# Kernel tuning notes

Hardware: AMD Instinct MI355X
Metric: run time of the kernel (lower is better)

Reference implementation:

```python
import jax, jax.numpy as jnp
import numpy as np

D_K = 64
EPS = 1e-6


def setup_inputs() -> dict:
    key = jax.random.key(0)
    ks = jax.random.split(key, 6)
    B, S, D2, DV = 4, 2048, 1024, 64
    q = jax.random.normal(ks[0], (B, S, D2), dtype=jnp.float32)
    k = jax.random.normal(ks[1], (B, S, D2), dtype=jnp.float32)
    v = jax.random.normal(ks[2], (B, S, D2), dtype=jnp.float32)
    mask = jax.random.randint(ks[3], (B, S, S), 0, 2) == 1
    V = jax.random.normal(ks[4], (1, DV), dtype=jnp.float32)
    fc_w = jax.random.normal(ks[5], (D2, DV), dtype=jnp.float32) * (1.0 / np.sqrt(DV))
    fc_b = jnp.zeros((D2,), dtype=jnp.float32)
    ln_g = jnp.ones((D2,), dtype=jnp.float32)
    ln_b = jnp.zeros((D2,), dtype=jnp.float32)
    return {"q": q, "k": k, "v": v, "mask": mask, "V": V,
            "fc_w": fc_w, "fc_b": fc_b, "ln_g": ln_g, "ln_b": ln_b}


def _layer_norm(x, g, b):
    mu = jnp.mean(x, axis=-1, keepdims=True)
    var = jnp.var(x, axis=-1, keepdims=True)
    return (x - mu) * jax.lax.rsqrt(var + EPS) * g + b


def reference(q, k, v, mask, V, fc_w, fc_b, ln_g, ln_b):
    residual = q
    qn = _layer_norm(q, ln_g, ln_b)
    # scaled dot-product scores (no softmax in this variant)
    attn = jnp.einsum('bsd,btd->bst', qn / jnp.sqrt(jnp.float32(D_K)), k)
    attn = jnp.where(mask, 0.0, attn)  # masked_fill with 0
    # v_ = V broadcast over (batch, seq, key); attn @ v_ == row-sum outer V
    output = jnp.sum(attn, axis=-1, keepdims=True) * V  # [B,S,d_v]
    output = output @ fc_w.T + fc_b                     # [B,S,2*d_model]
    output = output + residual
    return (output, attn)
```

## Files before the change

kernel.cpp:

```cpp
#include <hip/hip_runtime.h>
#include <hip/hip_bf16.h>
#include <cstdint>

#define S_LEN 2048
#define D2_   1024
#define DV_   64
#define NB_   4

typedef __bf16 bf16x8 __attribute__((ext_vector_type(8)));
typedef float  f32x4  __attribute__((ext_vector_type(4)));

__device__ __forceinline__ unsigned short f2bf(float f) {
  union { float f; unsigned int u; } v; v.f = f;
  unsigned int r = v.u + 0x7fffu + ((v.u >> 16) & 1u);
  return (unsigned short)(r >> 16);
}

__device__ __forceinline__ void async16(const unsigned short* g, unsigned short* l) {
  __builtin_amdgcn_global_load_lds(
      (__attribute__((address_space(1))) void*)g,
      (__attribute__((address_space(3))) void*)l,
      16, 0, 0);
}

__global__ void __launch_bounds__(256) ln_q_kernel(
    const float* __restrict__ q, const float* __restrict__ gam,
    const float* __restrict__ bet, unsigned short* __restrict__ qn) {
  const int row = blockIdx.x;
  const int t = threadIdx.x;
  const float4 x = ((const float4*)(q + (size_t)row * D2_))[t];
  float s  = x.x + x.y + x.z + x.w;
  float ss = x.x * x.x + x.y * x.y + x.z * x.z + x.w * x.w;
  #pragma unroll
  for (int o = 32; o > 0; o >>= 1) { s += __shfl_down(s, o); ss += __shfl_down(ss, o); }
  __shared__ float red[8];
  if ((t & 63) == 0) { red[t >> 6] = s; red[(t >> 6) + 4] = ss; }
  __syncthreads();
  const float tot  = red[0] + red[1] + red[2] + red[3];
  const float tots = red[4] + red[5] + red[6] + red[7];
  const float mu  = tot * (1.0f / D2_);
  const float var = tots * (1.0f / D2_) - mu * mu;
  const float rs  = rsqrtf(var + 1e-6f) * 0.125f;
  const float4 gv = ((const float4*)gam)[t];
  const float4 bv = ((const float4*)bet)[t];
  ushort4 o4;
  o4.x = f2bf((x.x - mu) * rs * gv.x + 0.125f * bv.x);
  o4.y = f2bf((x.y - mu) * rs * gv.y + 0.125f * bv.y);
  o4.z = f2bf((x.z - mu) * rs * gv.z + 0.125f * bv.z);
  o4.w = f2bf((x.w - mu) * rs * gv.w + 0.125f * bv.w);
  ((ushort4*)(qn + (size_t)row * D2_))[t] = o4;
}

__global__ void __launch_bounds__(256) cast_k_kernel(
    const float* __restrict__ k, unsigned short* __restrict__ kb) {
  const size_t i = ((size_t)blockIdx.x * 256 + threadIdx.x) * 8;
  const float4 a = ((const float4*)(k + i))[0];
  const float4 b = ((const float4*)(k + i))[1];
  ushort4 lo, hi;
  lo.x = f2bf(a.x); lo.y = f2bf(a.y); lo.z = f2bf(a.z); lo.w = f2bf(a.w);
  hi.x = f2bf(b.x); hi.y = f2bf(b.y); hi.z = f2bf(b.z); hi.w = f2bf(b.w);
  ((ushort4*)(kb + i))[0] = lo;
  ((ushort4*)(kb + i))[1] = hi;
}

__global__ void __launch_bounds__(256) w2_kernel(
    const float* __restrict__ V, const float* __restrict__ fw,
    float* __restrict__ w2) {
  const int d = blockIdx.x * 256 + threadIdx.x;
  const float4* r  = (const float4*)(fw + (size_t)d * DV_);
  const float4* vv = (const float4*)V;
  float s = 0.f;
  #pragma unroll
  for (int j = 0; j < 16; ++j) {
    const float4 a = r[j], b = vv[j];
    s += a.x * b.x + a.y * b.y + a.z * b.z + a.w * b.w;
  }
  w2[d] = s;
}

__global__ void __launch_bounds__(256) attn_gemm_kernel(
    const unsigned short* __restrict__ qn,
    const unsigned short* __restrict__ kb,
    const int* __restrict__ mask,
    float* __restrict__ attn) {
  __shared__ __align__(16) unsigned short Asm_[128 * 32];
  __shared__ __align__(16) unsigned short Bsm_[128 * 32];

  const int t  = threadIdx.x;
  const int bn = blockIdx.x * 128;
  const int bm = blockIdx.y * 128;
  const int bt = blockIdx.z;

  const unsigned short* gA = qn + ((size_t)bt * S_LEN + bm + (t >> 2)) * D2_ + (t & 3) * 8;
  const unsigned short* gB = kb + ((size_t)bt * S_LEN + bn + (t >> 2)) * D2_ + (t & 3) * 8;
  unsigned short* lA = Asm_ + t * 8;
  unsigned short* lB = Bsm_ + t * 8;

  const int lane = t & 63;
  const int w  = t >> 6;
  const int wm = (w >> 1) * 64;
  const int wn = (w & 1) * 64;
  const int lr = lane & 15;
  const int lg = lane >> 4;

  f32x4 acc[4][4] = {};

  for (int k0 = 0; k0 < D2_; k0 += 32) {
    async16(gA, lA);
    async16(gA + 64 * D2_, lA + 2048);
    async16(gB, lB);
    async16(gB + 64 * D2_, lB + 2048);
    gA += 32; gB += 32;
    __syncthreads();
    bf16x8 af[4], bfv[4];
    #pragma unroll
    for (int f = 0; f < 4; ++f) {
      af[f]  = *(const bf16x8*)(Asm_ + (wm + f * 16 + lr) * 32 + lg * 8);
      bfv[f] = *(const bf16x8*)(Bsm_ + (wn + f * 16 + lr) * 32 + lg * 8);
    }
    #pragma unroll
    for (int fm = 0; fm < 4; ++fm)
      #pragma unroll
      for (int fn = 0; fn < 4; ++fn)
        acc[fm][fn] = __builtin_amdgcn_mfma_f32_16x16x32_bf16(
            af[fm], bfv[fn], acc[fm][fn], 0, 0, 0);
    __syncthreads();
  }

  #pragma unroll
  for (int fm = 0; fm < 4; ++fm) {
    #pragma unroll
    for (int r = 0; r < 4; ++r) {
      const int srow = bm + wm + fm * 16 + lg * 4 + r;
      const size_t off = ((size_t)bt * S_LEN + srow) * S_LEN + bn + wn;
      const int* mrow = mask + off;
      float*    arow = attn + off;
      #pragma unroll
      for (int fn = 0; fn < 4; ++fn) {
        const int c = fn * 16 + lr;
        float vv = acc[fm][fn][r];
        vv = mrow[c] ? 0.0f : vv;
        arow[c] = vv;
      }
    }
  }
}

__global__ void __launch_bounds__(256) out_kernel(
    const float* __restrict__ attn, const float* __restrict__ q,
    const float* __restrict__ w2, const float* __restrict__ fcb,
    float* __restrict__ out) {
  const int row = blockIdx.x;
  const int t = threadIdx.x;
  const float4* ar = (const float4*)(attn + (size_t)row * S_LEN);
  const float4 a = ar[t], b = ar[t + 256];
  float s = a.x + a.y + a.z + a.w + b.x + b.y + b.z + b.w;
  #pragma unroll
  for (int o = 32; o > 0; o >>= 1) s += __shfl_down(s, o);
  __shared__ float red[4];
  if ((t & 63) == 0) red[t >> 6] = s;
  __syncthreads();
  const float rs = red[0] + red[1] + red[2] + red[3];
  const float4 wv = ((const float4*)w2)[t];
  const float4 bv = ((const float4*)fcb)[t];
  const float4 qv = ((const float4*)(q + (size_t)row * D2_))[t];
  float4 o4;
  o4.x = rs * wv.x + bv.x + qv.x;
  o4.y = rs * wv.y + bv.y + qv.y;
  o4.z = rs * wv.z + bv.z + qv.z;
  o4.w = rs * wv.w + bv.w + qv.w;
  ((float4*)(out + (size_t)row * D2_))[t] = o4;
}

extern "C" void kernel_launch(void* const* d_in, const int* in_sizes, int n_in,
                              void* d_out, int out_size, void* d_ws, size_t ws_size,
                              hipStream_t stream) {
  (void)in_sizes; (void)n_in; (void)out_size; (void)ws_size;
  const float* q    = (const float*)d_in[0];
  const float* k    = (const float*)d_in[1];
  const int*   mask = (const int*)d_in[3];
  const float* V    = (const float*)d_in[4];
  const float* fw   = (const float*)d_in[5];
  const float* fcb  = (const float*)d_in[6];
  const float* lg   = (const float*)d_in[7];
  const float* lb   = (const float*)d_in[8];

  float* out  = (float*)d_out;
  float* attn = out + (size_t)NB_ * S_LEN * D2_;

  unsigned short* qn = (unsigned short*)out;
  unsigned short* kb = qn + (size_t)NB_ * S_LEN * D2_;
  float* w2 = (float*)d_ws;

  ln_q_kernel<<<NB_ * S_LEN, 256, 0, stream>>>(q, lg, lb, qn);
  cast_k_kernel<<<(NB_ * S_LEN * D2_) / 2048, 256, 0, stream>>>(k, kb);
  w2_kernel<<<D2_ / 256, 256, 0, stream>>>(V, fw, w2);
  attn_gemm_kernel<<<dim3(S_LEN / 128, S_LEN / 128, NB_), 256, 0, stream>>>(qn, kb, mask, attn);
  out_kernel<<<NB_ * S_LEN, 256, 0, stream>>>(attn, q, w2, fcb, out);
}
```

Before: 297.3 us.

## Double-buffer LDS tiles in attention GEMM and fuse prep kernels

The attention GEMM now ping-pongs between two LDS buffers, issuing async global-to-LDS loads for the next K-slice before computing the current one, and drops the trailing barrier per iteration. The separate layernorm, K-cast and fc-weight-reduction kernels are merged into a single prep kernel to cut launches. This aims to hide global load latency behind MFMA work, at the cost of doubled LDS usage, which may reduce occupancy, and reliance on the barrier to drain the async loads.

```diff
diff --git a/kernel.cpp b/kernel.cpp
--- a/kernel.cpp
+++ b/kernel.cpp
@@ -23,11 +23,15 @@
       16, 0, 0);
 }
 
-__global__ void __launch_bounds__(256) ln_q_kernel(
-    const float* __restrict__ q, const float* __restrict__ gam,
-    const float* __restrict__ bet, unsigned short* __restrict__ qn) {
+__global__ void __launch_bounds__(256) prep_kernel(
+    const float* __restrict__ q, const float* __restrict__ k,
+    const float* __restrict__ gam, const float* __restrict__ bet,
+    const float* __restrict__ V, const float* __restrict__ fw,
+    unsigned short* __restrict__ qn, unsigned short* __restrict__ kb,
+    float* __restrict__ w2) {
   const int row = blockIdx.x;
   const int t = threadIdx.x;
+
   const float4 x = ((const float4*)(q + (size_t)row * D2_))[t];
   float s  = x.x + x.y + x.z + x.w;
   float ss = x.x * x.x + x.y * x.y + x.z * x.z + x.w * x.w;
@@ -49,33 +53,24 @@
   o4.z = f2bf((x.z - mu) * rs * gv.z + 0.125f * bv.z);
   o4.w = f2bf((x.w - mu) * rs * gv.w + 0.125f * bv.w);
   ((ushort4*)(qn + (size_t)row * D2_))[t] = o4;
-}
-
-__global__ void __launch_bounds__(256) cast_k_kernel(
-    const float* __restrict__ k, unsigned short* __restrict__ kb) {
-  const size_t i = ((size_t)blockIdx.x * 256 + threadIdx.x) * 8;
-  const float4 a = ((const float4*)(k + i))[0];
-  const float4 b = ((const float4*)(k + i))[1];
-  ushort4 lo, hi;
-  lo.x = f2bf(a.x); lo.y = f2bf(a.y); lo.z = f2bf(a.z); lo.w = f2bf(a.w);
-  hi.x = f2bf(b.x); hi.y = f2bf(b.y); hi.z = f2bf(b.z); hi.w = f2bf(b.w);
-  ((ushort4*)(kb + i))[0] = lo;
-  ((ushort4*)(kb + i))[1] = hi;
-}
-
-__global__ void __launch_bounds__(256) w2_kernel(
-    const float* __restrict__ V, const float* __restrict__ fw,
-    float* __restrict__ w2) {
-  const int d = blockIdx.x * 256 + threadIdx.x;
-  const float4* r  = (const float4*)(fw + (size_t)d * DV_);
-  const float4* vv = (const float4*)V;
-  float s = 0.f;
-  #pragma unroll
-  for (int j = 0; j < 16; ++j) {
-    const float4 a = r[j], b = vv[j];
-    s += a.x * b.x + a.y * b.y + a.z * b.z + a.w * b.w;
+
+  const float4 kx = ((const float4*)(k + (size_t)row * D2_))[t];
+  ushort4 k4;
+  k4.x = f2bf(kx.x); k4.y = f2bf(kx.y); k4.z = f2bf(kx.z); k4.w = f2bf(kx.w);
+  ((ushort4*)(kb + (size_t)row * D2_))[t] = k4;
+
+  if (row < 4) {
+    const int d = row * 256 + t;
+    const float4* r  = (const float4*)(fw + (size_t)d * DV_);
+    const float4* vv = (const float4*)V;
+    float acc = 0.f;
+    #pragma unroll
+    for (int j = 0; j < 16; ++j) {
+      const float4 a = r[j], b = vv[j];
+      acc += a.x * b.x + a.y * b.y + a.z * b.z + a.w * b.w;
+    }
+    w2[d] = acc;
   }
-  w2[d] = s;
 }
 
 __global__ void __launch_bounds__(256) attn_gemm_kernel(
@@ -83,8 +78,8 @@
     const unsigned short* __restrict__ kb,
     const int* __restrict__ mask,
     float* __restrict__ attn) {
-  __shared__ __align__(16) unsigned short Asm_[128 * 32];
-  __shared__ __align__(16) unsigned short Bsm_[128 * 32];
+  __shared__ __align__(16) unsigned short Asm_[2][128 * 32];
+  __shared__ __align__(16) unsigned short Bsm_[2][128 * 32];
 
   const int t  = threadIdx.x;
   const int bn = blockIdx.x * 128;
@@ -93,8 +88,6 @@
 
   const unsigned short* gA = qn + ((size_t)bt * S_LEN + bm + (t >> 2)) * D2_ + (t & 3) * 8;
   const unsigned short* gB = kb + ((size_t)bt * S_LEN + bn + (t >> 2)) * D2_ + (t & 3) * 8;
-  unsigned short* lA = Asm_ + t * 8;
-  unsigned short* lB = Bsm_ + t * 8;
 
   const int lane = t & 63;
   const int w  = t >> 6;
@@ -105,18 +98,31 @@
 
   f32x4 acc[4][4] = {};
 
-  for (int k0 = 0; k0 < D2_; k0 += 32) {
-    async16(gA, lA);
-    async16(gA + 64 * D2_, lA + 2048);
-    async16(gB, lB);
-    async16(gB + 64 * D2_, lB + 2048);
-    gA += 32; gB += 32;
+  async16(gA, Asm_[0] + t * 8);
+  async16(gA + 64 * D2_, Asm_[0] + t * 8 + 2048);
+  async16(gB, Bsm_[0] + t * 8);
+  async16(gB + 64 * D2_, Bsm_[0] + t * 8 + 2048);
+  gA += 32; gB += 32;
+
+  #pragma unroll 4
+  for (int it = 0; it < 32; ++it) {
     __syncthreads();
+    const unsigned short* Ac = Asm_[it & 1];
+    const unsigned short* Bc = Bsm_[it & 1];
+    if (it < 31) {
+      unsigned short* An = Asm_[(it + 1) & 1];
+      unsigned short* Bn = Bsm_[(it + 1) & 1];
+      async16(gA, An + t * 8);
+      async16(gA + 64 * D2_, An + t * 8 + 2048);
+      async16(gB, Bn + t * 8);
+      async16(gB + 64 * D2_, Bn + t * 8 + 2048);
+      gA += 32; gB += 32;
+    }
     bf16x8 af[4], bfv[4];
     #pragma unroll
     for (int f = 0; f < 4; ++f) {
-      af[f]  = *(const bf16x8*)(Asm_ + (wm + f * 16 + lr) * 32 + lg * 8);
-      bfv[f] = *(const bf16x8*)(Bsm_ + (wn + f * 16 + lr) * 32 + lg * 8);
+      af[f]  = *(const bf16x8*)(Ac + (wm + f * 16 + lr) * 32 + lg * 8);
+      bfv[f] = *(const bf16x8*)(Bc + (wn + f * 16 + lr) * 32 + lg * 8);
     }
     #pragma unroll
     for (int fm = 0; fm < 4; ++fm)
@@ -124,7 +130,6 @@
       for (int fn = 0; fn < 4; ++fn)
         acc[fm][fn] = __builtin_amdgcn_mfma_f32_16x16x32_bf16(
             af[fm], bfv[fn], acc[fm][fn], 0, 0, 0);
-    __syncthreads();
   }
 
   #pragma unroll
@@ -192,9 +197,7 @@
   unsigned short* kb = qn + (size_t)NB_ * S_LEN * D2_;
   float* w2 = (float*)d_ws;
 
-  ln_q_kernel<<<NB_ * S_LEN, 256, 0, stream>>>(q, lg, lb, qn);
-  cast_k_kernel<<<(NB_ * S_LEN * D2_) / 2048, 256, 0, stream>>>(k, kb);
-  w2_kernel<<<D2_ / 256, 256, 0, stream>>>(V, fw, w2);
+  prep_kernel<<<NB_ * S_LEN, 256, 0, stream>>>(q, k, lg, lb, V, fw, qn, kb, w2);
   attn_gemm_kernel<<<dim3(S_LEN / 128, S_LEN / 128, NB_), 256, 0, stream>>>(qn, kb, mask, attn);
   out_kernel<<<NB_ * S_LEN, 256, 0, stream>>>(attn, q, w2, fcb, out);
 }
```

New measurement: 295.6 us. About the same (-0.6%).
